# Kernel optimization log

Measured on AMD Instinct MI355X. Metric: run time of the kernel, lower is better.

The kernel has to match this reference:

```python
import jax, jax.numpy as jnp
import numpy as np
from jax import lax

HIDDEN_DIM = 256


def _conv(x, w, b, stride):
    # x: [B,T,H,W,Cin], w: [1,kh,kw,Cin,Cout]
    y = lax.conv_general_dilated(
        x, w, window_strides=(1, stride, stride), padding='SAME',
        dimension_numbers=('NDHWC', 'DHWIO', 'NDHWC'))
    return y + b


def _encode(video, w1, b1, w2, b2, w3, b3):
    x = video / 255.0
    x = jax.nn.relu(_conv(x, w1, b1, 2))
    x = jax.nn.relu(_conv(x, w2, b2, 2))
    x = jax.nn.relu(_conv(x, w3, b3, 2))
    return x  # [B,T,H/8,W/8,HIDDEN_DIM]


def _sample_features(features, t_idx, y_idx, x_idx):
    # Bilinear sample features[b, t_idx, y_idx, x_idx] -> [B,N,C]
    B, T, H, W, C = features.shape
    t = jnp.clip(t_idx, 0, T - 1)
    y0 = jnp.clip(jnp.floor(y_idx).astype(jnp.int32), 0, H - 1)
    y1 = jnp.clip(y0 + 1, 0, H - 1)
    x0 = jnp.clip(jnp.floor(x_idx).astype(jnp.int32), 0, W - 1)
    x1 = jnp.clip(x0 + 1, 0, W - 1)
    wy1 = y_idx - y0.astype(features.dtype)
    wy0 = 1.0 - wy1
    wx1 = x_idx - x0.astype(features.dtype)
    wx0 = 1.0 - wx1
    bi = jnp.arange(B)[:, None]
    f00 = features[bi, t, y0, x0]
    f01 = features[bi, t, y0, x1]
    f10 = features[bi, t, y1, x0]
    f11 = features[bi, t, y1, x1]
    f0 = f00 * wx0[..., None] + f01 * wx1[..., None]
    f1 = f10 * wx0[..., None] + f11 * wx1[..., None]
    return f0 * wy0[..., None] + f1 * wy1[..., None]


def _forward(video, query_points, w1, b1, w2, b2, w3, b3):
    B, T, H, W, _ = video.shape
    N = query_points.shape[1]
    x = _encode(video, w1, b1, w2, b2, w3, b3)
    feat_H, feat_W = x.shape[2], x.shape[3]
    query_t = (query_points[:, :, 0] * (T - 1)).astype(jnp.int32)
    query_y = query_points[:, :, 1] * (feat_H - 1)
    query_x = query_points[:, :, 2] * (feat_W - 1)
    q = _sample_features(x, query_t, query_y, query_x)  # [B,N,C]
    # dense correlation volume [B,N,T,fH,fW]
    corr = jnp.einsum('bnc,bthwc->bnthw', q, x) / jnp.sqrt(jnp.float32(HIDDEN_DIM))
    probs = jax.nn.softmax(corr.reshape(B, N, T, feat_H * feat_W) * 10.0, axis=-1)
    yy, xx = jnp.meshgrid(jnp.arange(feat_H, dtype=x.dtype),
                          jnp.arange(feat_W, dtype=x.dtype), indexing='ij')
    coords_flat = jnp.stack([xx.flatten(), yy.flatten()], axis=-1)  # [fH*fW, 2]
    pred = jnp.einsum('bntk,kc->bntc', probs, coords_flat)
    pred = pred.at[..., 0].set(pred[..., 0] * (W / feat_W))
    pred = pred.at[..., 1].set(pred[..., 1] * (H / feat_H))
    occlusion = jax.nn.sigmoid(-jnp.max(corr, axis=(-2, -1)))  # [B,N,T]
    return pred, occlusion


def setup_inputs() -> dict:
    key = jax.random.key(0)
    ks = jax.random.split(key, 10)
    B, T, H, W, N = 2, 24, 256, 256, 512
    video = jax.random.uniform(ks[0], (B, T, H, W, 3), jnp.float32) * 255.0
    query_points = jax.random.uniform(ks[1], (B, N, 3), jnp.float32)
    s = 0.05
    w1 = jax.random.normal(ks[2], (1, 7, 7, 3, 64), jnp.float32) * s
    b1 = jnp.zeros((64,), jnp.float32)
    w2 = jax.random.normal(ks[3], (1, 3, 3, 64, 128), jnp.float32) * s
    b2 = jnp.zeros((128,), jnp.float32)
    w3 = jax.random.normal(ks[4], (1, 3, 3, 128, HIDDEN_DIM), jnp.float32) * s
    b3 = jnp.zeros((HIDDEN_DIM,), jnp.float32)
    return {'video': video, 'query_points': query_points,
            'w1': w1, 'b1': b1, 'w2': w2, 'b2': b2, 'w3': w3, 'b3': b3}


def reference(video, query_points, w1, b1, w2, b2, w3, b3):
    return _forward(video, query_points, w1, b1, w2, b2, w3, b3)
```

## Files before the change

### kernel.cpp

```cpp
#include <hip/hip_runtime.h>
#include <hip/hip_bf16.h>
#include <cstdint>
#include <cstddef>


typedef __attribute__((ext_vector_type(8))) short bf16x8;
typedef __attribute__((ext_vector_type(4))) float f32x4;

typedef const __attribute__((address_space(1))) void gv_t;
typedef __attribute__((address_space(3))) void sv_t;

__device__ __forceinline__ unsigned short bfr(float f) {
    return (unsigned short)(__bfloat16_as_ushort(__float2bfloat16(f)));
}

__global__ __launch_bounds__(256) void k_prep(const float* __restrict__ video,
                                              const float* __restrict__ w1,
                                              const float* __restrict__ w2,
                                              const float* __restrict__ w3,
                                              __hip_bfloat16* __restrict__ pv,
                                              unsigned short* __restrict__ c1p,
                                              unsigned short* __restrict__ c2p,
                                              __hip_bfloat16* __restrict__ wp1,
                                              __hip_bfloat16* __restrict__ wp2,
                                              __hip_bfloat16* __restrict__ wp3)
{
    const int bid = blockIdx.x;
    if (bid < 12288) {
        const int iy = bid & 255;
        const int bt = bid >> 8;
        const int ix = threadIdx.x;
        const float* src = video + ((size_t)(bt * 256 + iy) * 256 + ix) * 3;
        unsigned* dst = (unsigned*)(pv + ((size_t)(bt * 261) + iy + 2) * 1056);
        const float v0 = src[0], v1 = src[1], v2 = src[2];
        const unsigned lo = (unsigned)bfr(v0) | ((unsigned)bfr(v1) << 16);
        const unsigned hi = (unsigned)bfr(v2);
        dst[(2 + ix) * 2 + 0] = lo;
        dst[(2 + ix) * 2 + 1] = hi;
        if (ix < 2)   { dst[ix * 2] = 0u; dst[ix * 2 + 1] = 0u; }
        if (ix >= 250){ dst[(ix + 8) * 2] = 0u; dst[(ix + 8) * 2 + 1] = 0u; }
    } else if (bid < 12288 + 7170) {
        const int i = (bid - 12288) * 256 + threadIdx.x;
        unsigned short* pvs = (unsigned short*)pv;
        if (i < 253440) {
            const int bt = i / 5280, rr = (i % 5280) / 1056, col = i % 1056;
            const int row = (rr < 2) ? rr : rr + 256;
            pvs[(size_t)(bt * 261 + row) * 1056 + col] = 0;
        } else if (i < 1042944) {
            const int j = i - 253440, bt = j / 16448, k = j % 16448;
            size_t addr;
            if (k < 8256) { const int px = k >> 6, c = k & 63;
                addr = ((size_t)(bt * 129 + 128) * 129 + px) * 64 + c; }
            else { const int k2 = k - 8256, row = k2 >> 6, c = k2 & 63;
                addr = ((size_t)(bt * 129 + row) * 129 + 128) * 64 + c; }
            c1p[addr] = 0;
        } else if (i < 1835520) {
            const int j = i - 1042944, bt = j / 16512, k = j % 16512;
            size_t addr;
            if (k < 8320) { const int px = k >> 7, c = k & 127;
                addr = ((size_t)(bt * 65 + 64) * 65 + px) * 128 + c; }
            else { const int k2 = k - 8320, row = k2 >> 7, c = k2 & 127;
                addr = ((size_t)(bt * 65 + row) * 65 + 64) * 128 + c; }
            c2p[addr] = 0;
        }
    } else {
        const int e = (bid - 12288 - 7170) * 256 + threadIdx.x;
        if (e < 14336) {
            const int j = e & 7, lane = (e >> 3) & 63, nt = (e >> 9) & 3, kh = e >> 11;
            const int k = ((lane >> 4) << 3) + j;
            const int kw = k >> 2, ci = k & 3;
            const int n = nt * 16 + (lane & 15);
            float v = (ci < 3 && kw < 7) ? w1[(size_t)((kh * 7 + kw) * 3 + ci) * 64 + n] : 0.f;
            wp1[e] = __float2bfloat16(v);
        } else if (e < 88064) {
            const int e2 = e - 14336;
            const int j = e2 & 7, lane = (e2 >> 3) & 63, nt = (e2 >> 9) & 7, ks = (e2 >> 12) & 1, tap = e2 >> 13;
            const int ci = ks * 32 + ((lane >> 4) << 3) + j;
            const int n  = nt * 16 + (lane & 15);
            wp2[e2] = __float2bfloat16(w2[(size_t)(tap * 64 + ci) * 128 + n]);
        } else {
            const int e3 = e - 88064;
            const int j = e3 & 7, lane = (e3 >> 3) & 63, nt = (e3 >> 9) & 15, ks = (e3 >> 13) & 3, tap = e3 >> 15;
            const int ci = ks * 32 + ((lane >> 4) << 3) + j;
            const int n  = nt * 16 + (lane & 15);
            wp3[e3] = __float2bfloat16(w3[(size_t)(tap * 128 + ci) * 256 + n]);
        }
    }
}

__global__ __launch_bounds__(256) void k_conv1m(const __hip_bfloat16* __restrict__ pv,
                                                const __hip_bfloat16* __restrict__ wp,
                                                const float* __restrict__ b1,
                                                __hip_bfloat16* __restrict__ out)
{
    const int xcd = blockIdx.x & 7;
    const int sub = blockIdx.x >> 3;
    const int bt  = xcd * 6 + (sub >> 7);
    const int oy  = sub & 127;
    const int w  = threadIdx.x >> 6;
    const int l  = threadIdx.x & 63;
    const int li = l & 15, lh = l >> 4;

    f32x4 acc[2][4];
#pragma unroll
    for (int m = 0; m < 2; ++m)
#pragma unroll
        for (int n = 0; n < 4; ++n) acc[m][n] = (f32x4){0.f, 0.f, 0.f, 0.f};

    const short* pvS = (const short*)pv;
    const short* wS  = (const short*)wp;

#pragma unroll
    for (int kh = 0; kh < 7; ++kh) {
        const short* row = pvS + (size_t)(bt * 261 + oy * 2 + kh) * 1056;
        bf16x8 bw[4];
#pragma unroll
        for (int nt = 0; nt < 4; ++nt)
            bw[nt] = *reinterpret_cast<const bf16x8*>(wS + ((size_t)(kh * 4 + nt) * 64 + l) * 8);
#pragma unroll
        for (int mt = 0; mt < 2; ++mt) {
            const int ox = w * 32 + mt * 16 + li;
            bf16x8 a = *reinterpret_cast<const bf16x8*>(row + 8 * (ox + lh));
#pragma unroll
            for (int nt = 0; nt < 4; ++nt)
                acc[mt][nt] = __builtin_amdgcn_mfma_f32_16x16x32_bf16(a, bw[nt], acc[mt][nt], 0, 0, 0);
        }
    }

    __hip_bfloat16* op = out + ((size_t)(bt * 129 + oy) * 129) * 64;
#pragma unroll
    for (int mt = 0; mt < 2; ++mt) {
        const int px0 = w * 32 + mt * 16 + lh * 4;
#pragma unroll
        for (int nt = 0; nt < 4; ++nt) {
            const int n = nt * 16 + li;
            const float bias = b1[n];
#pragma unroll
            for (int r = 0; r < 4; ++r) {
                const float v = fmaxf(acc[mt][nt][r] * (1.f / 255.f) + bias, 0.f);
                op[(size_t)(px0 + r) * 64 + n] = __float2bfloat16(v);
            }
        }
    }
}

template<int CIN, int COUT, int OW, int IW, int ORS>
__global__ __launch_bounds__(256, 3) void k_convg(const __hip_bfloat16* __restrict__ in,
                                                  const __hip_bfloat16* __restrict__ wp,
                                                  const float* __restrict__ bias,
                                                  __hip_bfloat16* __restrict__ out)
{
    constexpr int KSN = CIN / 32;
    constexpr int NSL = 9 * KSN;
    constexpr int NTT = COUT / 16;
    constexpr int XT  = OW / 16;
    constexpr int RPB = 128 / OW;
    constexpr int MTB = (OW * OW) / 128;
    constexpr int NH  = COUT / 128;
    constexpr int PARTS = MTB * NH;

    __shared__ char lbuf[3][16384];

    const int bid  = blockIdx.x;
    const int xcd  = bid & 7;
    const int sub  = bid >> 3;
    const int grp  = sub / PARTS;
    const int part = sub % PARTS;
    const int bt   = xcd * 6 + grp;
    const int mblk = part % MTB;
    const int nh   = part / MTB;

    const int tid = threadIdx.x;
    const int w   = tid >> 6;
    const int l   = tid & 63;
    const int li  = l & 15, lh = l >> 4;
    const int mw  = w >> 1, nw = w & 1;

    const int oy0  = mblk * RPB;
    const int roy0 = oy0 * 2;

    const short* inS = (const short*)in + (size_t)bt * IW * IW * CIN;
    const char*  wB  = (const char*)wp + (size_t)(nh * 8) * 1024;

    const int g0 = tid, g1 = tid + 256;
    const int q0 = g0 >> 7, px0_ = g0 & 127;
    const int q1 = g1 >> 7, px1_ = g1 & 127;
    const short* aA0 = inS + ((size_t)(roy0 + ((px0_ >> 4) / XT) * 2) * IW
                              + ((px0_ >> 4) % XT) * 32 + (px0_ & 15) * 2) * CIN + q0 * 8;
    const short* aA1 = inS + ((size_t)(roy0 + ((px1_ >> 4) / XT) * 2) * IW
                              + ((px1_ >> 4) % XT) * 32 + (px1_ & 15) * 2) * CIN + q1 * 8;

    f32x4 acc[4][4];
#pragma unroll
    for (int i = 0; i < 4; ++i)
#pragma unroll
        for (int j = 0; j < 4; ++j) acc[i][j] = (f32x4){0.f, 0.f, 0.f, 0.f};

    auto stage = [&](int S, int B) {
        const int tap = S / KSN, ks = S % KSN;
        const int kh = tap / 3, kw = tap % 3;
        const int ao = (kh * IW + kw) * CIN + ks * 32;
        char* dst = &lbuf[B][0];
        __builtin_amdgcn_global_load_lds((gv_t*)(aA0 + ao), (sv_t*)(dst + g0 * 16), 16, 0, 0);
        __builtin_amdgcn_global_load_lds((gv_t*)(aA1 + ao), (sv_t*)(dst + g1 * 16), 16, 0, 0);
        const char* bs = wB + (size_t)S * (NTT * 1024) + tid * 16;
        __builtin_amdgcn_global_load_lds((gv_t*)(bs),        (sv_t*)(dst + 8192 + tid * 16), 16, 0, 0);
        __builtin_amdgcn_global_load_lds((gv_t*)(bs + 4096), (sv_t*)(dst + 12288 + tid * 16), 16, 0, 0);
    };

    stage(0, 0);
    stage(1, 1);
    asm volatile("s_waitcnt vmcnt(4)" ::: "memory");
    __builtin_amdgcn_sched_barrier(0);
    __builtin_amdgcn_s_barrier();
    __builtin_amdgcn_sched_barrier(0);

#pragma unroll
    for (int s = 0; s < NSL; ++s) {
        if (s + 2 < NSL) stage(s + 2, (s + 2) % 3);

        const char* bufc = &lbuf[s % 3][0];
        bf16x8 af[4], bf[4];
#pragma unroll
        for (int i = 0; i < 4; ++i)
            af[i] = *reinterpret_cast<const bf16x8*>(bufc + lh * 2048 + (mw * 4 + i) * 256 + li * 16);
#pragma unroll
        for (int j = 0; j < 4; ++j)
            bf[j] = *reinterpret_cast<const bf16x8*>(bufc + 8192 + (nw * 4 + j) * 1024 + l * 16);

#pragma unroll
        for (int i = 0; i < 4; ++i)
#pragma unroll
            for (int j = 0; j < 4; ++j)
                acc[i][j] = __builtin_amdgcn_mfma_f32_16x16x32_bf16(af[i], bf[j], acc[i][j], 0, 0, 0);

        if (s + 1 < NSL) {
            if (s + 2 < NSL) asm volatile("s_waitcnt vmcnt(4)" ::: "memory");
            else             asm volatile("s_waitcnt vmcnt(0)" ::: "memory");
            __builtin_amdgcn_sched_barrier(0);
            __builtin_amdgcn_s_barrier();
            __builtin_amdgcn_sched_barrier(0);
        }
    }

    __hip_bfloat16* ob = out + (size_t)bt * ORS * ORS * COUT;
#pragma unroll
    for (int i = 0; i < 4; ++i) {
        const int mt  = mw * 4 + i;
        const int oy  = oy0 + mt / XT;
        const int oxb = (mt % XT) * 16 + lh * 4;
#pragma unroll
        for (int j = 0; j < 4; ++j) {
            const int n = (nh * 8 + nw * 4 + j) * 16 + li;
            const float bv = bias[n];
#pragma unroll
            for (int r = 0; r < 4; ++r) {
                const float v = fmaxf(acc[i][j][r] + bv, 0.f);
                ob[((size_t)oy * ORS + oxb + r) * COUT + n] = __float2bfloat16(v);
            }
        }
    }
}

__global__ __launch_bounds__(256) void k_sample(const float* __restrict__ qp,
                                                const __hip_bfloat16* __restrict__ feat,
                                                __hip_bfloat16* __restrict__ q)
{
    const int bn = blockIdx.x;
    const int b  = bn >> 9;
    const float t3 = qp[bn * 3 + 0];
    const float yv = qp[bn * 3 + 1] * 31.f;
    const float xv = qp[bn * 3 + 2] * 31.f;
    int t = (int)(t3 * 23.f);
    t = min(max(t, 0), 23);
    int y0 = (int)floorf(yv); y0 = min(max(y0, 0), 31);
    const int y1 = min(y0 + 1, 31);
    int x0 = (int)floorf(xv); x0 = min(max(x0, 0), 31);
    const int x1 = min(x0 + 1, 31);
    const float wy1 = yv - (float)y0, wy0 = 1.f - wy1;
    const float wx1 = xv - (float)x0, wx0 = 1.f - wx1;

    const int c = threadIdx.x;
    const __hip_bfloat16* fb = feat + ((size_t)(b * 24 + t) * 1024) * 256;
    const float f00 = __bfloat162float(fb[(size_t)(y0 * 32 + x0) * 256 + c]);
    const float f01 = __bfloat162float(fb[(size_t)(y0 * 32 + x1) * 256 + c]);
    const float f10 = __bfloat162float(fb[(size_t)(y1 * 32 + x0) * 256 + c]);
    const float f11 = __bfloat162float(fb[(size_t)(y1 * 32 + x1) * 256 + c]);
    const float v = (f00 * wx0 + f01 * wx1) * wy0 + (f10 * wx0 + f11 * wx1) * wy1;
    q[(size_t)bn * 256 + c] = __float2bfloat16(v);
}

__global__ __launch_bounds__(256, 2) void k_corrm(const __hip_bfloat16* __restrict__ qb,
                                                  const __hip_bfloat16* __restrict__ featb,
                                                  float* __restrict__ pbuf)
{
    __shared__ short lbuf[2][8192];

    const int bid = blockIdx.x;
    const int xcd = bid & 7;
    const int sub = bid >> 3;
    const int grp = sub >> 5;
    const int prt = sub & 31;
    const int img = xcd * 6 + grp;
    const int bq  = img / 24, t = img % 24;
    const int nc  = prt & 3, ps = prt >> 2;

    const int tid = threadIdx.x;
    const int w   = tid >> 6;
    const int l   = tid & 63;
    const int li  = l & 15, lh = l >> 4;

    const short* qS = (const short*)qb;
    const short* fS = (const short*)featb + (size_t)img * 1024 * 256;
    const char*  tile0 = (const char*)(fS + (size_t)(ps * 128) * 256);

    const int q0 = nc * 128 + w * 32;
    bf16x8 aq[2][8];
#pragma unroll
    for (int mt = 0; mt < 2; ++mt)
#pragma unroll
        for (int ks = 0; ks < 8; ++ks)
            aq[mt][ks] = *reinterpret_cast<const bf16x8*>(
                qS + ((size_t)(bq * 512 + q0 + mt * 16 + li)) * 256 + ks * 32 + lh * 8);

    float m[2][4], s[2][4], sx[2][4], sy[2][4], dmx[2][4];
#pragma unroll
    for (int mt = 0; mt < 2; ++mt)
#pragma unroll
        for (int r = 0; r < 4; ++r) {
            m[mt][r] = -1e30f; s[mt][r] = 0.f; sx[mt][r] = 0.f; sy[mt][r] = 0.f; dmx[mt][r] = -1e30f;
        }

    bf16x8 stg[4];
#pragma unroll
    for (int i = 0; i < 4; ++i) {
        const int g = i * 256 + tid;
        const int pos = g >> 5, kb = (g & 31) * 16;
        stg[i] = *reinterpret_cast<const bf16x8*>(tile0 + (size_t)pos * 512 + kb);
    }
#pragma unroll
    for (int i = 0; i < 4; ++i) {
        const int g = i * 256 + tid;
        const int pos = g >> 5, kb = (g & 31) * 16;
        *reinterpret_cast<bf16x8*>((char*)&lbuf[0][0] + pos * 512 + (kb ^ ((pos & 7) << 4))) = stg[i];
    }
    __syncthreads();

#pragma unroll
    for (int st = 0; st < 4; ++st) {
        const int cur = st & 1;

        if (st < 3) {
            const char* tn = tile0 + (size_t)((st + 1) * 32) * 512;
#pragma unroll
            for (int i = 0; i < 4; ++i) {
                const int g = i * 256 + tid;
                const int pos = g >> 5, kb = (g & 31) * 16;
                stg[i] = *reinterpret_cast<const bf16x8*>(tn + (size_t)pos * 512 + kb);
            }
        }

        f32x4 acc[2][2];
#pragma unroll
        for (int mt = 0; mt < 2; ++mt)
#pragma unroll
            for (int pt = 0; pt < 2; ++pt) acc[mt][pt] = (f32x4){0.f, 0.f, 0.f, 0.f};

#pragma unroll
        for (int pt = 0; pt < 2; ++pt) {
            const int p = pt * 16 + li;
#pragma unroll
            for (int ks = 0; ks < 8; ++ks) {
                const int k = ks * 32 + lh * 8;
                bf16x8 bv = *reinterpret_cast<const bf16x8*>(&lbuf[cur][p * 256 + (k ^ ((p & 7) << 3))]);
                acc[0][pt] = __builtin_amdgcn_mfma_f32_16x16x32_bf16(aq[0][ks], bv, acc[0][pt], 0, 0, 0);
                acc[1][pt] = __builtin_amdgcn_mfma_f32_16x16x32_bf16(aq[1][ks], bv, acc[1][pt], 0, 0, 0);
            }
        }

        const float py = (float)(ps * 4 + st);
#pragma unroll
        for (int mt = 0; mt < 2; ++mt)
#pragma unroll
            for (int r = 0; r < 4; ++r) {
                const float v0 = acc[mt][0][r], v1 = acc[mt][1][r];
                float mx = fmaxf(v0, v1);
                mx = fmaxf(mx, __shfl_xor(mx, 1));
                mx = fmaxf(mx, __shfl_xor(mx, 2));
                mx = fmaxf(mx, __shfl_xor(mx, 4));
                mx = fmaxf(mx, __shfl_xor(mx, 8));
                dmx[mt][r] = fmaxf(dmx[mt][r], mx);
                const float mn = fmaxf(m[mt][r], mx * 0.625f);
                const float sc = __expf(m[mt][r] - mn);
                const float e0 = __expf(v0 * 0.625f - mn);
                const float e1 = __expf(v1 * 0.625f - mn);
                const float es = e0 + e1;
                s[mt][r]  = s[mt][r]  * sc + es;
                sx[mt][r] = sx[mt][r] * sc + es * (float)li + 16.f * e1;
                sy[mt][r] = sy[mt][r] * sc + es * py;
                m[mt][r] = mn;
            }

        if (st < 3) {
#pragma unroll
            for (int i = 0; i < 4; ++i) {
                const int g = i * 256 + tid;
                const int pos = g >> 5, kb = (g & 31) * 16;
                *reinterpret_cast<bf16x8*>((char*)&lbuf[cur ^ 1][0] + pos * 512 + (kb ^ ((pos & 7) << 4))) = stg[i];
            }
            __syncthreads();
        }
    }

#pragma unroll
    for (int mt = 0; mt < 2; ++mt)
#pragma unroll
        for (int r = 0; r < 4; ++r) {
#pragma unroll
            for (int off = 1; off < 16; off <<= 1) {
                s[mt][r]  += __shfl_xor(s[mt][r],  off);
                sx[mt][r] += __shfl_xor(sx[mt][r], off);
                sy[mt][r] += __shfl_xor(sy[mt][r], off);
            }
        }

    if (li == 0) {
#pragma unroll
        for (int mt = 0; mt < 2; ++mt)
#pragma unroll
            for (int r = 0; r < 4; ++r) {
                const int n = q0 + mt * 16 + lh * 4 + r;
                const int bnt = (bq * 512 + n) * 24 + t;
                const int pi = ps * 24576 + bnt;
                pbuf[pi]                = m[mt][r];
                pbuf[196608 + pi]       = s[mt][r];
                pbuf[393216 + pi]       = sx[mt][r];
                pbuf[589824 + pi]       = sy[mt][r];
                pbuf[786432 + pi]       = dmx[mt][r];
            }
    }
}

__global__ __launch_bounds__(256) void k_merge(const float* __restrict__ pbuf,
                                               float* __restrict__ outp)
{
    const int i = blockIdx.x * 256 + threadIdx.x;
    float M = -1e30f, D = -1e30f;
#pragma unroll
    for (int ps = 0; ps < 8; ++ps) {
        M = fmaxf(M, pbuf[ps * 24576 + i]);
        D = fmaxf(D, pbuf[786432 + ps * 24576 + i]);
    }
    float s = 0.f, sx = 0.f, sy = 0.f;
#pragma unroll
    for (int ps = 0; ps < 8; ++ps) {
        const int pi = ps * 24576 + i;
        const float wgt = __expf(pbuf[pi] - M);
        s  += pbuf[196608 + pi] * wgt;
        sx += pbuf[393216 + pi] * wgt;
        sy += pbuf[589824 + pi] * wgt;
    }
    const float inv = 8.f / s;
    outp[i * 2 + 0] = sx * inv;
    outp[i * 2 + 1] = sy * inv;
    outp[49152 + i] = 1.f / (1.f + __expf(D * 0.0625f));
}

extern "C" void kernel_launch(void* const* d_in, const int* in_sizes, int n_in,
                              void* d_out, int out_size, void* d_ws, size_t ws_size,
                              hipStream_t stream)
{
    const float* video = (const float*)d_in[0];
    const float* qp    = (const float*)d_in[1];
    const float* w1    = (const float*)d_in[2];
    const float* b1    = (const float*)d_in[3];
    const float* w2    = (const float*)d_in[4];
    const float* b2    = (const float*)d_in[5];
    const float* w3    = (const float*)d_in[6];
    const float* b3    = (const float*)d_in[7];
    float* out = (float*)d_out;

    char* wsb = (char*)d_ws;
    __hip_bfloat16* c1p   = (__hip_bfloat16*)(wsb);
    __hip_bfloat16* c2p   = (__hip_bfloat16*)(wsb + 102242304ull);
    __hip_bfloat16* pv    = (__hip_bfloat16*)(wsb + 154159104ull);
    __hip_bfloat16* featb = (__hip_bfloat16*)(wsb + 154159104ull);
    __hip_bfloat16* qbuf  = (__hip_bfloat16*)(wsb + 180618240ull);
    __hip_bfloat16* w1p   = (__hip_bfloat16*)(wsb + 181142528ull);
    __hip_bfloat16* w2p   = (__hip_bfloat16*)(wsb + 181171200ull);
    __hip_bfloat16* w3p   = (__hip_bfloat16*)(wsb + 181318656ull);
    float*          pbuf  = (float*)(wsb + 181908480ull);

    k_prep      <<<dim3(20954),    dim3(256), 0, stream>>>(
                       video, w1, w2, w3, pv,
                       (unsigned short*)c1p, (unsigned short*)c2p, w1p, w2p, w3p);
    k_conv1m    <<<dim3(48 * 128), dim3(256), 0, stream>>>(pv, w1p, b1, c1p);
    k_convg<64, 128, 64, 129, 65><<<dim3(1536), dim3(256), 0, stream>>>(c1p, w2p, b2, c2p);
    k_convg<128, 256, 32, 65, 32><<<dim3(768),  dim3(256), 0, stream>>>(c2p, w3p, b3, featb);
    k_sample    <<<dim3(1024),     dim3(256), 0, stream>>>(qp, featb, qbuf);
    k_corrm     <<<dim3(1536),     dim3(256), 0, stream>>>(qbuf, featb, pbuf);
    k_merge     <<<dim3(96),       dim3(256), 0, stream>>>(pbuf, out);
}
```

Baseline: 197.0 us.

## Restructure stride-2 convs to stage input rows once in swizzled LDS

Replaces the per-slice triple-buffered conv pipeline with a kernel where each block handles one output row. The block loads its three input rows into LDS once with an XOR swizzle and reuses them across all 9 taps, while weights are read directly from global memory into registers. This removes the repeated per-tap A-tile staging and the per-slice barriers, at the cost of smaller per-block tiles (2x4 MFMA tiles per wave), more blocks, and uncached-in-LDS weight reads that now rely on L1/L2.

```diff
diff --git a/kernel.cpp b/kernel.cpp
--- a/kernel.cpp
+++ b/kernel.cpp
@@ -144,119 +144,99 @@
     }
 }
 
-template<int CIN, int COUT, int OW, int IW, int ORS>
-__global__ __launch_bounds__(256, 3) void k_convg(const __hip_bfloat16* __restrict__ in,
+template<int CIN, int COUT, int OW, int IW, int ORS, int NWN>
+__global__ __launch_bounds__(256, 3) void k_convr(const __hip_bfloat16* __restrict__ in,
                                                   const __hip_bfloat16* __restrict__ wp,
                                                   const float* __restrict__ bias,
                                                   __hip_bfloat16* __restrict__ out)
 {
-    constexpr int KSN = CIN / 32;
-    constexpr int NSL = 9 * KSN;
-    constexpr int NTT = COUT / 16;
-    constexpr int XT  = OW / 16;
-    constexpr int RPB = 128 / OW;
-    constexpr int MTB = (OW * OW) / 128;
-    constexpr int NH  = COUT / 128;
-    constexpr int PARTS = MTB * NH;
-
-    __shared__ char lbuf[3][16384];
-
-    const int bid  = blockIdx.x;
-    const int xcd  = bid & 7;
-    const int sub  = bid >> 3;
-    const int grp  = sub / PARTS;
-    const int part = sub % PARTS;
-    const int bt   = xcd * 6 + grp;
-    const int mblk = part % MTB;
-    const int nh   = part / MTB;
+    constexpr int KSN  = CIN / 32;
+    constexpr int NSL  = 9 * KSN;
+    constexpr int NTT  = COUT / 16;
+    constexpr int GPX  = CIN / 8;
+    constexpr int ROWG = IW * GPX;
+    constexpr int RST  = ROWG * 16;
+    constexpr int TOT  = 3 * ROWG;
+
+    __shared__ char lbuf[3 * RST];
+
+    const int bid = blockIdx.x;
+    const int xcd = bid & 7;
+    const int sub = bid >> 3;
+    const int bt  = xcd * 6 + sub / OW;
+    const int oy  = sub % OW;
 
     const int tid = threadIdx.x;
     const int w   = tid >> 6;
     const int l   = tid & 63;
     const int li  = l & 15, lh = l >> 4;
-    const int mw  = w >> 1, nw = w & 1;
-
-    const int oy0  = mblk * RPB;
-    const int roy0 = oy0 * 2;
-
-    const short* inS = (const short*)in + (size_t)bt * IW * IW * CIN;
-    const char*  wB  = (const char*)wp + (size_t)(nh * 8) * 1024;
-
-    const int g0 = tid, g1 = tid + 256;
-    const int q0 = g0 >> 7, px0_ = g0 & 127;
-    const int q1 = g1 >> 7, px1_ = g1 & 127;
-    const short* aA0 = inS + ((size_t)(roy0 + ((px0_ >> 4) / XT) * 2) * IW
-                              + ((px0_ >> 4) % XT) * 32 + (px0_ & 15) * 2) * CIN + q0 * 8;
-    const short* aA1 = inS + ((size_t)(roy0 + ((px1_ >> 4) / XT) * 2) * IW
-                              + ((px1_ >> 4) % XT) * 32 + (px1_ & 15) * 2) * CIN + q1 * 8;
-
-    f32x4 acc[4][4];
-#pragma unroll
-    for (int i = 0; i < 4; ++i)
+    const int mt0 = (w / NWN) * 2;
+    const int ntb = (w % NWN) * 4;
+
+    const short* inS = (const short*)in;
+    const size_t rb = (size_t)(bt * IW + oy * 2) * IW * CIN;
+#pragma unroll
+    for (int it = 0; it < 13; ++it) {
+        const int g = it * 256 + tid;
+        if (g < TOT) {
+            const int r  = g / ROWG;
+            const int rm = g - r * ROWG;
+            const int px = rm / GPX;
+            const int j  = rm - px * GPX;
+            const int q  = j ^ ((px >> 1) & 7);
+            __builtin_amdgcn_global_load_lds(
+                (gv_t*)(inS + rb + (size_t)r * IW * CIN + px * CIN + q * 8),
+                (sv_t*)(lbuf + (size_t)g * 16), 16, 0, 0);
+        }
+    }
+    __syncthreads();
+
+    f32x4 acc[2][4];
+#pragma unroll
+    for (int i = 0; i < 2; ++i)
 #pragma unroll
         for (int j = 0; j < 4; ++j) acc[i][j] = (f32x4){0.f, 0.f, 0.f, 0.f};
 
-    auto stage = [&](int S, int B) {
-        const int tap = S / KSN, ks = S % KSN;
+    const char* wB = (const char*)wp;
+
+#pragma unroll
+    for (int s = 0; s < NSL; ++s) {
+        const int tap = s / KSN, ks = s % KSN;
         const int kh = tap / 3, kw = tap % 3;
-        const int ao = (kh * IW + kw) * CIN + ks * 32;
-        char* dst = &lbuf[B][0];
-        __builtin_amdgcn_global_load_lds((gv_t*)(aA0 + ao), (sv_t*)(dst + g0 * 16), 16, 0, 0);
-        __builtin_amdgcn_global_load_lds((gv_t*)(aA1 + ao), (sv_t*)(dst + g1 * 16), 16, 0, 0);
-        const char* bs = wB + (size_t)S * (NTT * 1024) + tid * 16;
-        __builtin_amdgcn_global_load_lds((gv_t*)(bs),        (sv_t*)(dst + 8192 + tid * 16), 16, 0, 0);
-        __builtin_amdgcn_global_load_lds((gv_t*)(bs + 4096), (sv_t*)(dst + 12288 + tid * 16), 16, 0, 0);
-    };
-
-    stage(0, 0);
-    stage(1, 1);
-    asm volatile("s_waitcnt vmcnt(4)" ::: "memory");
-    __builtin_amdgcn_sched_barrier(0);
-    __builtin_amdgcn_s_barrier();
-    __builtin_amdgcn_sched_barrier(0);
-
-#pragma unroll
-    for (int s = 0; s < NSL; ++s) {
-        if (s + 2 < NSL) stage(s + 2, (s + 2) % 3);
-
-        const char* bufc = &lbuf[s % 3][0];
-        bf16x8 af[4], bf[4];
-#pragma unroll
-        for (int i = 0; i < 4; ++i)
-            af[i] = *reinterpret_cast<const bf16x8*>(bufc + lh * 2048 + (mw * 4 + i) * 256 + li * 16);
+
+        bf16x8 bf[4];
 #pragma unroll
         for (int j = 0; j < 4; ++j)
-            bf[j] = *reinterpret_cast<const bf16x8*>(bufc + 8192 + (nw * 4 + j) * 1024 + l * 16);
-
-#pragma unroll
-        for (int i = 0; i < 4; ++i)
+            bf[j] = *reinterpret_cast<const bf16x8*>(wB + ((size_t)s * NTT + ntb + j) * 1024 + l * 16);
+
+        const char* Ar = lbuf + kh * RST;
+        bf16x8 af[2];
+#pragma unroll
+        for (int i = 0; i < 2; ++i) {
+            const int ix  = ((mt0 + i) * 16 + li) * 2 + kw;
+            const int off = ((ks * 4 + lh) ^ ((ix >> 1) & 7)) * 16;
+            af[i] = *reinterpret_cast<const bf16x8*>(Ar + (size_t)ix * (CIN * 2) + off);
+        }
+
+#pragma unroll
+        for (int i = 0; i < 2; ++i)
 #pragma unroll
             for (int j = 0; j < 4; ++j)
                 acc[i][j] = __builtin_amdgcn_mfma_f32_16x16x32_bf16(af[i], bf[j], acc[i][j], 0, 0, 0);
-
-        if (s + 1 < NSL) {
-            if (s + 2 < NSL) asm volatile("s_waitcnt vmcnt(4)" ::: "memory");
-            else             asm volatile("s_waitcnt vmcnt(0)" ::: "memory");
-            __builtin_amdgcn_sched_barrier(0);
-            __builtin_amdgcn_s_barrier();
-            __builtin_amdgcn_sched_barrier(0);
-        }
-    }
-
-    __hip_bfloat16* ob = out + (size_t)bt * ORS * ORS * COUT;
-#pragma unroll
-    for (int i = 0; i < 4; ++i) {
-        const int mt  = mw * 4 + i;
-        const int oy  = oy0 + mt / XT;
-        const int oxb = (mt % XT) * 16 + lh * 4;
+    }
+
+    __hip_bfloat16* ob = out + (size_t)(bt * ORS + oy) * ORS * COUT;
+#pragma unroll
+    for (int i = 0; i < 2; ++i) {
+        const int ox = (mt0 + i) * 16 + lh * 4;
 #pragma unroll
         for (int j = 0; j < 4; ++j) {
-            const int n = (nh * 8 + nw * 4 + j) * 16 + li;
+            const int n = (ntb + j) * 16 + li;
             const float bv = bias[n];
 #pragma unroll
             for (int r = 0; r < 4; ++r) {
                 const float v = fmaxf(acc[i][j][r] + bv, 0.f);
-                ob[((size_t)oy * ORS + oxb + r) * COUT + n] = __float2bfloat16(v);
+                ob[(size_t)(ox + r) * COUT + n] = __float2bfloat16(v);
             }
         }
     }
@@ -495,8 +475,8 @@
                        video, w1, w2, w3, pv,
                        (unsigned short*)c1p, (unsigned short*)c2p, w1p, w2p, w3p);
     k_conv1m    <<<dim3(48 * 128), dim3(256), 0, stream>>>(pv, w1p, b1, c1p);
-    k_convg<64, 128, 64, 129, 65><<<dim3(1536), dim3(256), 0, stream>>>(c1p, w2p, b2, c2p);
-    k_convg<128, 256, 32, 65, 32><<<dim3(768),  dim3(256), 0, stream>>>(c2p, w3p, b3, featb);
+    k_convr<64, 128, 64, 129, 65, 2><<<dim3(3072), dim3(256), 0, stream>>>(c1p, w2p, b2, c2p);
+    k_convr<128, 256, 32, 65, 32, 4><<<dim3(1536), dim3(256), 0, stream>>>(c2p, w3p, b3, featb);
     k_sample    <<<dim3(1024),     dim3(256), 0, stream>>>(qp, featb, qbuf);
     k_corrm     <<<dim3(1536),     dim3(256), 0, stream>>>(qbuf, featb, pbuf);
     k_merge     <<<dim3(96),       dim3(256), 0, stream>>>(pbuf, out);
```

New measurement: 196.9 us. No clear change (-0.0%).
